# Kernel tuning notes

Measured on AMD Instinct MI355X. Metric: run time of the kernel, lower is better.

## Reference

```python
import jax, jax.numpy as jnp
import numpy as np

B = 4096          # players (batch)
DEG = 64          # asteroids per player
A = B * DEG       # total asteroids
E = A             # one edge per asteroid (asteroid -> its player)
PD, AD, ED = 5, 3, 7
HID = 64
HEADS = 4
OUT = HID         # GATv2Conv out_channels (concat=False -> mean over heads)
L = 2             # num_layers
NEG_SLOPE = 0.2
LN_EPS = 1e-5


def setup_inputs() -> dict:
    key = jax.random.key(0)
    ks = jax.random.split(key, 20)
    f = jnp.float32
    inp = {}
    inp["player_feat"] = jax.random.normal(ks[0], (B, PD), f)
    inp["asteroid_feat"] = jax.random.normal(ks[1], (A, AD), f)
    src = jnp.arange(E, dtype=jnp.int32)
    dst = src // DEG                      # player batch index per edge
    inp["edge_index"] = jnp.stack([src, dst])  # [2, E] int32
    inp["edge_attr"] = jax.random.normal(ks[2], (E, ED), f)
    sc = 0.1
    # input projections
    inp["Wp"] = jax.random.normal(ks[3], (PD, HID), f) * sc
    inp["bp"] = jnp.zeros((HID,), f)
    inp["Wa"] = jax.random.normal(ks[4], (AD, HID), f) * sc
    inp["ba"] = jnp.zeros((HID,), f)
    # per-layer GATv2 params (stacked over L)
    inp["Wl"] = jax.random.normal(ks[5], (L, HID, HEADS * OUT), f) * sc
    inp["bl"] = jnp.zeros((L, HEADS * OUT), f)
    inp["Wr"] = jax.random.normal(ks[6], (L, HID, HEADS * OUT), f) * sc
    inp["br"] = jnp.zeros((L, HEADS * OUT), f)
    inp["We"] = jax.random.normal(ks[7], (L, ED, HEADS * OUT), f) * sc
    inp["att"] = jax.random.normal(ks[8], (L, HEADS, OUT), f) * sc
    inp["bias"] = jnp.zeros((L, OUT), f)
    inp["ln_g"] = jnp.ones((L, HID), f)
    inp["ln_b"] = jnp.zeros((L, HID), f)
    return inp


def _layer_norm(x, g, b):
    mu = jnp.mean(x, axis=-1, keepdims=True)
    var = jnp.mean(jnp.square(x - mu), axis=-1, keepdims=True)
    return (x - mu) * jax.lax.rsqrt(var + LN_EPS) * g + b


def _gatv2(x, src, dst, edge_attr, Wl, bl, Wr, br, We, att, bias, n_nodes):
    # x: [N, HID]; src/dst: [E]; PyG GATv2Conv, add_self_loops=False, concat=False
    xl = (x @ Wl + bl).reshape(-1, HEADS, OUT)   # source transform
    xr = (x @ Wr + br).reshape(-1, HEADS, OUT)   # target transform
    ea = (edge_attr @ We).reshape(-1, HEADS, OUT)
    e = xl[src] + xr[dst] + ea                   # [E, H, O]
    e = jnp.where(e >= 0, e, NEG_SLOPE * e)      # LeakyReLU(0.2)
    logits = jnp.einsum('eho,ho->eh', e, att)    # [E, H]
    # segment softmax over incoming edges of each target node
    m = jax.ops.segment_max(logits, dst, num_segments=n_nodes)
    al = jnp.exp(logits - m[dst])
    den = jax.ops.segment_sum(al, dst, num_segments=n_nodes)
    alpha = al / den[dst]                        # [E, H]
    msg = alpha[:, :, None] * xl[src]            # [E, H, O]
    out = jax.ops.segment_sum(msg, dst, num_segments=n_nodes)  # [N, H, O]
    return jnp.mean(out, axis=1) + bias          # concat=False -> head mean


def reference(player_feat, asteroid_feat, edge_index, edge_attr,
              Wp, bp, Wa, ba, Wl, bl, Wr, br, We, att, bias, ln_g, ln_b):
    batch = player_feat.shape[0]
    h_p = jax.nn.relu(player_feat @ Wp + bp)
    h_a = jax.nn.relu(asteroid_feat @ Wa + ba)
    x = jnp.concatenate([h_p, h_a], axis=0)      # [N, HID]
    n_nodes = x.shape[0]
    src = edge_index[0] + batch                  # asteroid local -> global idx
    dst = edge_index[1]
    for i in range(L):
        x_new = _gatv2(x, src, dst, edge_attr, Wl[i], bl[i], Wr[i], br[i],
                       We[i], att[i], bias[i], n_nodes)
        x = _layer_norm(x + jax.nn.relu(x_new), ln_g[i], ln_b[i])
    return x[:batch]
```

## Files before the change

kernel.cpp:

```cpp
#include <hip/hip_runtime.h>


typedef __bf16 bf16x8 __attribute__((ext_vector_type(8)));
typedef float  f32x4  __attribute__((ext_vector_type(4)));

union FragU { unsigned short u[8]; bf16x8 v; };

__device__ __forceinline__ float bf2f(unsigned short u) {
    union { unsigned int i; float f; } v; v.i = ((unsigned int)u) << 16; return v.f;
}
__device__ __forceinline__ unsigned short f2bf(float f) {
    union { __bf16 b; unsigned short u; } x; x.b = (__bf16)f; return x.u;
}

#define NEG_SLOPE 0.2f
#define LN_EPS 1e-5f
#define XS 88

struct Smem {
    __align__(16) unsigned short xa[2][64 * XS];
    __align__(16) unsigned short xpb[2][64];
    __align__(16) float alf[2][256];
    float outp[2][256];
    float xp[2][64];
    float afs[2][192];
    float rbs[64], gs[64], bs[64];
};

#define WS_NEED (163840 + 3 * 8192)

__global__ __launch_bounds__(256) void prep_weights(
    const float* __restrict__ Wl, const float* __restrict__ Wr,
    const float* __restrict__ We, const float* __restrict__ bl,
    const float* __restrict__ att, const float* __restrict__ br,
    unsigned short* __restrict__ wlf, unsigned short* __restrict__ wrf,
    unsigned short* __restrict__ wef, f32x4* __restrict__ blq,
    f32x4* __restrict__ attq, f32x4* __restrict__ brq)
{
    int s = blockIdx.x * 256 + threadIdx.x;
    {
        int layer = s >> 14, k = (s >> 8) & 63, c = s & 255;
        int jj = k & 7, q = (k >> 3) & 3, ko = k >> 5;
        int nt = (c >> 4) & 3, frag = nt * 2 + ko;
        int t = (c >> 6) * 64 + q * 16 + (c & 15);
        int di = ((layer * 8 + frag) * 256 + t) * 8 + jj;
        wlf[di] = f2bf(Wl[s]);
        wrf[di] = f2bf(Wr[s]);
    }
    int i = s;
    if (i < 16384) {
        int j2 = i & 7, t2 = (i >> 3) & 255, n2 = (i >> 11) & 3, l2 = (i >> 13) & 1;
        int q2 = (t2 >> 4) & 3;
        int c2 = (t2 >> 6) * 64 + n2 * 16 + (t2 & 15);
        wef[i] = (q2 == 0 && j2 < 7) ? f2bf(We[l2 * 1792 + j2 * 256 + c2])
                                     : (unsigned short)0;
    }
    if (i < 512) {
        int lyr = i >> 8, tt = i & 255;
        int hb = (tt >> 6) * 64, mm = tt & 15;
        f32x4 b, a, r;
        #pragma unroll
        for (int n = 0; n < 4; ++n) {
            int cc = hb + n * 16 + mm;
            b[n] = bl[lyr * 256 + cc];
            a[n] = att[lyr * 256 + cc];
            r[n] = br[lyr * 256 + cc];
        }
        blq[i] = b; attq[i] = a; brq[i] = r;
    }
}

template <bool WS>
__global__ __launch_bounds__(256) void gnn_main(
    const float* __restrict__ pf, const float* __restrict__ af,
    const float* __restrict__ eat, const float* __restrict__ Wp,
    const float* __restrict__ bp, const float* __restrict__ Wa,
    const float* __restrict__ ba, const float* __restrict__ Wl,
    const float* __restrict__ bl, const float* __restrict__ Wr,
    const float* __restrict__ br, const float* __restrict__ We,
    const float* __restrict__ att, const float* __restrict__ bias,
    const float* __restrict__ lng, const float* __restrict__ lnb,
    const unsigned short* __restrict__ wlf, const unsigned short* __restrict__ wrf,
    const unsigned short* __restrict__ wef, const f32x4* __restrict__ blq,
    const f32x4* __restrict__ attq, const f32x4* __restrict__ brq,
    float* __restrict__ out)
{
    __shared__ Smem sm;
    const int p0 = blockIdx.x * 2, t = threadIdx.x;
    const int w = t >> 6, l = t & 63, q = l >> 4, m = l & 15;
    const int cbase = w * 64;

    #pragma unroll
    for (int idx = t; idx < 384; idx += 256) {
        int pl = idx >= 192, o = idx - pl * 192;
        sm.afs[pl][o] = af[(p0 + pl) * 192 + o];
    }
    if (t < 64) {
        sm.rbs[t] = fmaxf(bias[t], 0.f);
        sm.gs[t] = lng[t];
        sm.bs[t] = lnb[t];
    }
    if (t < 128) {
        int pl = t >> 6, tt = t & 63;
        float acc = bp[tt];
        #pragma unroll
        for (int d = 0; d < 5; ++d) acc += pf[(p0 + pl) * 5 + d] * Wp[d * 64 + tt];
        float xp0 = fmaxf(acc, 0.f);
        sm.xp[pl][tt] = xp0;
        sm.xpb[pl][tt] = f2bf(xp0);
    }
    __syncthreads();
    {
        const int pl = w >> 1, rbase = (w & 1) * 32, k = l;
        float wa0 = Wa[k], wa1 = Wa[64 + k], wa2 = Wa[128 + k], bak = ba[k];
        #pragma unroll
        for (int rep = 0; rep < 32; ++rep) {
            int j = rbase + rep;
            float acc = bak + sm.afs[pl][j * 3] * wa0 + sm.afs[pl][j * 3 + 1] * wa1
                      + sm.afs[pl][j * 3 + 2] * wa2;
            sm.xa[pl][j * XS + k] = f2bf(fmaxf(acc, 0.f));
        }
    }
    #pragma unroll
    for (int idx = t; idx < 1024; idx += 256) {
        int pl = idx >> 9, jd = idx & 511, j = jd >> 3, d = jd & 7;
        sm.xa[pl][j * XS + 64 + d] = (d < 7) ? f2bf(eat[((p0 + pl) * 64 + j) * 7 + d])
                                             : (unsigned short)0;
    }
    __syncthreads();

    for (int layer = 0; layer < 2; ++layer) {
        f32x4 blv, atv, brv;
        if constexpr (WS) {
            blv = blq[layer * 256 + t];
            atv = attq[layer * 256 + t];
            brv = brq[layer * 256 + t];
        } else {
            #pragma unroll
            for (int nt = 0; nt < 4; ++nt) {
                int c = cbase + nt * 16 + m;
                blv[nt] = bl[layer * 256 + c];
                atv[nt] = att[layer * 256 + c];
                brv[nt] = br[layer * 256 + c];
            }
        }

        float xrc[2][4];
        {
            FragU xf0[2], xf1[2];
            #pragma unroll
            for (int pl = 0; pl < 2; ++pl) {
                xf0[pl].v = *reinterpret_cast<const bf16x8*>(&sm.xpb[pl][q * 8]);
                xf1[pl].v = *reinterpret_cast<const bf16x8*>(&sm.xpb[pl][32 + q * 8]);
            }
            #pragma unroll
            for (int nt = 0; nt < 4; ++nt) {
                FragU r0, r1;
                if constexpr (WS) {
                    r0.v = *reinterpret_cast<const bf16x8*>(&wrf[((layer * 8 + nt * 2 + 0) * 256 + t) * 8]);
                    r1.v = *reinterpret_cast<const bf16x8*>(&wrf[((layer * 8 + nt * 2 + 1) * 256 + t) * 8]);
                } else {
                    int c = cbase + nt * 16 + m;
                    #pragma unroll
                    for (int jj = 0; jj < 8; ++jj) {
                        r0.u[jj] = f2bf(Wr[layer * 16384 + (q * 8 + jj) * 256 + c]);
                        r1.u[jj] = f2bf(Wr[layer * 16384 + (32 + q * 8 + jj) * 256 + c]);
                    }
                }
                #pragma unroll
                for (int pl = 0; pl < 2; ++pl) {
                    f32x4 cx = { brv[nt], brv[nt], brv[nt], brv[nt] };
                    cx = __builtin_amdgcn_mfma_f32_16x16x32_bf16(xf0[pl].v, r0.v, cx, 0, 0, 0);
                    cx = __builtin_amdgcn_mfma_f32_16x16x32_bf16(xf1[pl].v, r1.v, cx, 0, 0, 0);
                    xrc[pl][nt] = cx[0];
                }
            }
        }

        FragU bfr[8];
        bf16x8 ebf[4];
        if constexpr (WS) {
            #pragma unroll
            for (int f = 0; f < 8; ++f)
                bfr[f].v = *reinterpret_cast<const bf16x8*>(&wlf[((layer * 8 + f) * 256 + t) * 8]);
            #pragma unroll
            for (int nt = 0; nt < 4; ++nt)
                ebf[nt] = *reinterpret_cast<const bf16x8*>(&wef[((layer * 4 + nt) * 256 + t) * 8]);
        } else {
            const float* Wli = Wl + layer * 16384;
            #pragma unroll
            for (int nt = 0; nt < 4; ++nt) {
                int c = cbase + nt * 16 + m;
                #pragma unroll
                for (int ko = 0; ko < 2; ++ko) {
                    int kb = ko * 32 + q * 8;
                    #pragma unroll
                    for (int jj = 0; jj < 8; ++jj)
                        bfr[nt * 2 + ko].u[jj] = f2bf(Wli[(kb + jj) * 256 + c]);
                }
                FragU e;
                #pragma unroll
                for (int jj = 0; jj < 8; ++jj)
                    e.u[jj] = (q == 0 && jj < 7) ? f2bf(We[layer * 1792 + jj * 256 + c])
                                                 : (unsigned short)0;
                ebf[nt] = e.v;
            }
        }

        float bx[2][4];
        #pragma unroll
        for (int pl = 0; pl < 2; ++pl)
            #pragma unroll
            for (int nt = 0; nt < 4; ++nt) bx[pl][nt] = blv[nt] + xrc[pl][nt];

        const bool b0 = (m & 1) != 0, b1 = (m & 2) != 0;
        const bool b2 = (m & 4) != 0, b3 = (m & 8) != 0;
        float P[2][4];
        #pragma unroll
        for (int mt = 0; mt < 4; ++mt) {
            const int row = mt * 16 + m;
            #pragma unroll
            for (int pl = 0; pl < 2; ++pl) {
                bf16x8 a0 = *reinterpret_cast<const bf16x8*>(&sm.xa[pl][row * XS + q * 8]);
                bf16x8 a1 = *reinterpret_cast<const bf16x8*>(&sm.xa[pl][row * XS + 32 + q * 8]);
                bf16x8 a2 = *reinterpret_cast<const bf16x8*>(&sm.xa[pl][row * XS + 64]);
                float lp4[4] = { 0.f, 0.f, 0.f, 0.f };
                #pragma unroll
                for (int nt = 0; nt < 4; ++nt) {
                    f32x4 acc = { bx[pl][nt], bx[pl][nt], bx[pl][nt], bx[pl][nt] };
                    acc = __builtin_amdgcn_mfma_f32_16x16x32_bf16(a0, bfr[nt * 2 + 0].v, acc, 0, 0, 0);
                    acc = __builtin_amdgcn_mfma_f32_16x16x32_bf16(a1, bfr[nt * 2 + 1].v, acc, 0, 0, 0);
                    f32x4 ef = __builtin_amdgcn_mfma_f32_16x16x32_bf16(a2, ebf[nt], acc, 0, 0, 0);
                    #pragma unroll
                    for (int r = 0; r < 4; ++r) {
                        float ev = ef[r];
                        ev = fmaxf(ev, NEG_SLOPE * ev);
                        lp4[r] += ev * atv[nt];
                    }
                }
                float e0k = b0 ? lp4[1] : lp4[0], e0s = b0 ? lp4[0] : lp4[1];
                float ea = e0k + __shfl_xor(e0s, 1, 64);
                float e1k = b0 ? lp4[3] : lp4[2], e1s = b0 ? lp4[2] : lp4[3];
                float eb = e1k + __shfl_xor(e1s, 1, 64);
                float fk = b1 ? eb : ea, fs = b1 ? ea : eb;
                P[pl][mt] = fk + __shfl_xor(fs, 2, 64);
            }
        }

        float rden[2];
        #pragma unroll
        for (int pl = 0; pl < 2; ++pl) {
            float g0k = b2 ? P[pl][1] : P[pl][0], g0s = b2 ? P[pl][0] : P[pl][1];
            float ga = g0k + __shfl_xor(g0s, 4, 64);
            float g1k = b2 ? P[pl][3] : P[pl][2], g1s = b2 ? P[pl][2] : P[pl][3];
            float gb = g1k + __shfl_xor(g1s, 4, 64);
            float hk = b3 ? gb : ga, hs = b3 ? ga : gb;
            float lg = hk + __shfl_xor(hs, 8, 64);
            float al = __expf(lg);
            float den = al;
            #pragma unroll
            for (int msk = 1; msk <= 32; msk <<= 1) den += __shfl_xor(den, msk, 64);
            rden[pl] = 1.f / den;
            const int rj = ((m >> 2) * 16) + (q * 4) + (m & 3);
            sm.alf[pl][w * 64 + rj] = al;
        }
        __builtin_amdgcn_wave_barrier();

        #pragma unroll
        for (int pl = 0; pl < 2; ++pl) {
            const f32x4* alv = reinterpret_cast<const f32x4*>(&sm.alf[pl][cbase]);
            f32x4 al4[4];
            #pragma unroll
            for (int mt = 0; mt < 4; ++mt) al4[mt] = alv[mt * 4 + q];
            float s[4] = { 0.f, 0.f, 0.f, 0.f };
            #pragma unroll
            for (int mt = 0; mt < 4; ++mt) {
                const int row = mt * 16 + m;
                bf16x8 a0 = *reinterpret_cast<const bf16x8*>(&sm.xa[pl][row * XS + q * 8]);
                bf16x8 a1 = *reinterpret_cast<const bf16x8*>(&sm.xa[pl][row * XS + 32 + q * 8]);
                #pragma unroll
                for (int nt = 0; nt < 4; ++nt) {
                    f32x4 c1 = { bx[pl][nt], bx[pl][nt], bx[pl][nt], bx[pl][nt] };
                    c1 = __builtin_amdgcn_mfma_f32_16x16x32_bf16(a0, bfr[nt * 2 + 0].v, c1, 0, 0, 0);
                    c1 = __builtin_amdgcn_mfma_f32_16x16x32_bf16(a1, bfr[nt * 2 + 1].v, c1, 0, 0, 0);
                    s[nt] += al4[mt][0] * c1[0] + al4[mt][1] * c1[1]
                           + al4[mt][2] * c1[2] + al4[mt][3] * c1[3];
                }
            }
            #pragma unroll
            for (int nt = 0; nt < 4; ++nt) {
                float sv = s[nt];
                sv += __shfl_xor(sv, 16, 64);
                sv += __shfl_xor(sv, 32, 64);
                if (q == 0) sm.outp[pl][cbase + nt * 16 + m] = sv * rden[pl] - xrc[pl][nt];
            }
        }
        __syncthreads();

        if (layer == 0) {
            {
                const int g = t >> 1, pl = g >> 6, j = g & 63, part = t & 1;
                unsigned short* rowp = &sm.xa[pl][j * XS + part * 32];
                FragU A0, A1, A2, A3;
                A0.v = *reinterpret_cast<const bf16x8*>(rowp);
                A1.v = *reinterpret_cast<const bf16x8*>(rowp + 8);
                A2.v = *reinterpret_cast<const bf16x8*>(rowp + 16);
                A3.v = *reinterpret_cast<const bf16x8*>(rowp + 24);
                float v[32], sum = 0.f, sq = 0.f;
                #pragma unroll
                for (int i = 0; i < 32; ++i) {
                    unsigned short us = (i < 8) ? A0.u[i] : (i < 16) ? A1.u[i - 8]
                                      : (i < 24) ? A2.u[i - 16] : A3.u[i - 24];
                    float x = bf2f(us) + sm.rbs[part * 32 + i];
                    v[i] = x; sum += x; sq += x * x;
                }
                sum += __shfl_xor(sum, 1, 64); sq += __shfl_xor(sq, 1, 64);
                float mu = sum * (1.f / 64.f);
                float var = sq * (1.f / 64.f) - mu * mu;
                float rs = rsqrtf(var + LN_EPS);
                FragU O0, O1, O2, O3;
                #pragma unroll
                for (int i = 0; i < 32; ++i) {
                    int col = part * 32 + i;
                    unsigned short ub = f2bf((v[i] - mu) * rs * sm.gs[col] + sm.bs[col]);
                    if (i < 8) O0.u[i] = ub;
                    else if (i < 16) O1.u[i - 8] = ub;
                    else if (i < 24) O2.u[i - 16] = ub;
                    else O3.u[i - 24] = ub;
                }
                *reinterpret_cast<bf16x8*>(rowp) = O0.v;
                *reinterpret_cast<bf16x8*>(rowp + 8) = O1.v;
                *reinterpret_cast<bf16x8*>(rowp + 16) = O2.v;
                *reinterpret_cast<bf16x8*>(rowp + 24) = O3.v;
            }
            if (t < 128) {
                const int pl = t >> 6, tt = t & 63;
                float xnew = 0.25f * (sm.outp[pl][tt] + sm.outp[pl][64 + tt]
                                    + sm.outp[pl][128 + tt] + sm.outp[pl][192 + tt])
                           + bias[tt];
                float v = sm.xp[pl][tt] + fmaxf(xnew, 0.f);
                float sum = v, sq = v * v;
                #pragma unroll
                for (int msk = 1; msk <= 32; msk <<= 1) {
                    sum += __shfl_xor(sum, msk, 64);
                    sq  += __shfl_xor(sq,  msk, 64);
                }
                float mu = sum * (1.f / 64.f);
                float var = sq * (1.f / 64.f) - mu * mu;
                float y = (v - mu) * rsqrtf(var + LN_EPS) * lng[tt] + lnb[tt];
                sm.xp[pl][tt] = y;
                sm.xpb[pl][tt] = f2bf(y);
            }
            __syncthreads();
        } else {
            if (t < 128) {
                const int pl = t >> 6, tt = t & 63;
                float xnew = 0.25f * (sm.outp[pl][tt] + sm.outp[pl][64 + tt]
                                    + sm.outp[pl][128 + tt] + sm.outp[pl][192 + tt])
                           + bias[64 + tt];
                float v = sm.xp[pl][tt] + fmaxf(xnew, 0.f);
                float sum = v, sq = v * v;
                #pragma unroll
                for (int msk = 1; msk <= 32; msk <<= 1) {
                    sum += __shfl_xor(sum, msk, 64);
                    sq  += __shfl_xor(sq,  msk, 64);
                }
                float mu = sum * (1.f / 64.f);
                float var = sq * (1.f / 64.f) - mu * mu;
                float y = (v - mu) * rsqrtf(var + LN_EPS) * lng[64 + tt] + lnb[64 + tt];
                out[(p0 + pl) * 64 + tt] = y;
            }
        }
    }
}

extern "C" void kernel_launch(void* const* d_in, const int* in_sizes, int n_in,
                              void* d_out, int out_size, void* d_ws, size_t ws_size,
                              hipStream_t stream) {
    const float* pf   = (const float*)d_in[0];
    const float* af   = (const float*)d_in[1];
    const float* eat  = (const float*)d_in[3];
    const float* Wp   = (const float*)d_in[4];
    const float* bp   = (const float*)d_in[5];
    const float* Wa   = (const float*)d_in[6];
    const float* ba   = (const float*)d_in[7];
    const float* Wl   = (const float*)d_in[8];
    const float* bl   = (const float*)d_in[9];
    const float* Wr   = (const float*)d_in[10];
    const float* br   = (const float*)d_in[11];
    const float* We   = (const float*)d_in[12];
    const float* att  = (const float*)d_in[13];
    const float* bias = (const float*)d_in[14];
    const float* lng  = (const float*)d_in[15];
    const float* lnb  = (const float*)d_in[16];
    float* out = (float*)d_out;

    const int B = in_sizes[0] / 5;
    unsigned short* wlf = (unsigned short*)d_ws;
    unsigned short* wrf = wlf + 32768;
    unsigned short* wef = wrf + 32768;
    f32x4* blq  = (f32x4*)((char*)d_ws + 163840);
    f32x4* attq = blq + 512;
    f32x4* brq  = attq + 512;

    if (ws_size >= WS_NEED) {
        prep_weights<<<dim3(128), dim3(256), 0, stream>>>(
            Wl, Wr, We, bl, att, br, wlf, wrf, wef, blq, attq, brq);
        gnn_main<true><<<dim3(B / 2), dim3(256), 0, stream>>>(
            pf, af, eat, Wp, bp, Wa, ba, Wl, bl, Wr, br, We, att, bias, lng, lnb,
            wlf, wrf, wef, blq, attq, brq, out);
    } else {
        gnn_main<false><<<dim3(B / 2), dim3(256), 0, stream>>>(
            pf, af, eat, Wp, bp, Wa, ba, Wl, bl, Wr, br, We, att, bias, lng, lnb,
            wlf, wrf, wef, blq, attq, brq, out);
    }
}
```

Before: 166.0 us.

## Process four players per block to amortize weight fragment loads

Each block now handles four players instead of two, so every weight fragment loaded from global memory feeds twice as many MFMA tiles, and the grid halves to B/4 blocks. The shared-memory row stride drops from 88 to 72, the per-row layer norm is done by one thread over 64 columns instead of two threads over 32, and launch bounds request 3 blocks per CU. In exchange, register pressure rises (64-float arrays, 4x4 accumulators), shared memory per block doubles, and the new stride may change LDS bank conflicts.

```diff
diff --git a/kernel.cpp b/kernel.cpp
--- a/kernel.cpp
+++ b/kernel.cpp
@@ -15,15 +15,15 @@
 
 #define NEG_SLOPE 0.2f
 #define LN_EPS 1e-5f
-#define XS 88
+#define XS 72
 
 struct Smem {
-    __align__(16) unsigned short xa[2][64 * XS];
-    __align__(16) unsigned short xpb[2][64];
-    __align__(16) float alf[2][256];
-    float outp[2][256];
-    float xp[2][64];
-    float afs[2][192];
+    __align__(16) unsigned short xa[4][64 * XS];
+    __align__(16) unsigned short xpb[4][64];
+    __align__(16) float alf[4][256];
+    float outp[4][256];
+    float xp[4][64];
+    float afs[4][192];
     float rbs[64], gs[64], bs[64];
 };
 
@@ -71,7 +71,7 @@
 }
 
 template <bool WS>
-__global__ __launch_bounds__(256) void gnn_main(
+__global__ __launch_bounds__(256, 3) void gnn_main(
     const float* __restrict__ pf, const float* __restrict__ af,
     const float* __restrict__ eat, const float* __restrict__ Wp,
     const float* __restrict__ bp, const float* __restrict__ Wa,
@@ -86,13 +86,14 @@
     float* __restrict__ out)
 {
     __shared__ Smem sm;
-    const int p0 = blockIdx.x * 2, t = threadIdx.x;
+    const int p0 = blockIdx.x * 4, t = threadIdx.x;
     const int w = t >> 6, l = t & 63, q = l >> 4, m = l & 15;
     const int cbase = w * 64;
 
     #pragma unroll
-    for (int idx = t; idx < 384; idx += 256) {
-        int pl = idx >= 192, o = idx - pl * 192;
+    for (int it = 0; it < 3; ++it) {
+        int idx = it * 256 + t;
+        int pl = idx / 192, o = idx - pl * 192;
         sm.afs[pl][o] = af[(p0 + pl) * 192 + o];
     }
     if (t < 64) {
@@ -100,8 +101,8 @@
         sm.gs[t] = lng[t];
         sm.bs[t] = lnb[t];
     }
-    if (t < 128) {
-        int pl = t >> 6, tt = t & 63;
+    {
+        int pl = w, tt = l;
         float acc = bp[tt];
         #pragma unroll
         for (int d = 0; d < 5; ++d) acc += pf[(p0 + pl) * 5 + d] * Wp[d * 64 + tt];
@@ -111,18 +112,18 @@
     }
     __syncthreads();
     {
-        const int pl = w >> 1, rbase = (w & 1) * 32, k = l;
+        const int pl = w, k = l;
         float wa0 = Wa[k], wa1 = Wa[64 + k], wa2 = Wa[128 + k], bak = ba[k];
         #pragma unroll
-        for (int rep = 0; rep < 32; ++rep) {
-            int j = rbase + rep;
+        for (int j = 0; j < 64; ++j) {
             float acc = bak + sm.afs[pl][j * 3] * wa0 + sm.afs[pl][j * 3 + 1] * wa1
                       + sm.afs[pl][j * 3 + 2] * wa2;
             sm.xa[pl][j * XS + k] = f2bf(fmaxf(acc, 0.f));
         }
     }
     #pragma unroll
-    for (int idx = t; idx < 1024; idx += 256) {
+    for (int it = 0; it < 8; ++it) {
+        int idx = it * 256 + t;
         int pl = idx >> 9, jd = idx & 511, j = jd >> 3, d = jd & 7;
         sm.xa[pl][j * XS + 64 + d] = (d < 7) ? f2bf(eat[((p0 + pl) * 64 + j) * 7 + d])
                                              : (unsigned short)0;
@@ -145,11 +146,11 @@
             }
         }
 
-        float xrc[2][4];
+        float bx[4][4];
         {
-            FragU xf0[2], xf1[2];
-            #pragma unroll
-            for (int pl = 0; pl < 2; ++pl) {
+            FragU xf0[4], xf1[4];
+            #pragma unroll
+            for (int pl = 0; pl < 4; ++pl) {
                 xf0[pl].v = *reinterpret_cast<const bf16x8*>(&sm.xpb[pl][q * 8]);
                 xf1[pl].v = *reinterpret_cast<const bf16x8*>(&sm.xpb[pl][32 + q * 8]);
             }
@@ -168,11 +169,11 @@
                     }
                 }
                 #pragma unroll
-                for (int pl = 0; pl < 2; ++pl) {
+                for (int pl = 0; pl < 4; ++pl) {
                     f32x4 cx = { brv[nt], brv[nt], brv[nt], brv[nt] };
                     cx = __builtin_amdgcn_mfma_f32_16x16x32_bf16(xf0[pl].v, r0.v, cx, 0, 0, 0);
                     cx = __builtin_amdgcn_mfma_f32_16x16x32_bf16(xf1[pl].v, r1.v, cx, 0, 0, 0);
-                    xrc[pl][nt] = cx[0];
+                    bx[pl][nt] = blv[nt] + cx[0];
                 }
             }
         }
@@ -207,20 +208,14 @@
             }
         }
 
-        float bx[2][4];
-        #pragma unroll
-        for (int pl = 0; pl < 2; ++pl)
-            #pragma unroll
-            for (int nt = 0; nt < 4; ++nt) bx[pl][nt] = blv[nt] + xrc[pl][nt];
-
         const bool b0 = (m & 1) != 0, b1 = (m & 2) != 0;
         const bool b2 = (m & 4) != 0, b3 = (m & 8) != 0;
-        float P[2][4];
+        float P[4][4];
         #pragma unroll
         for (int mt = 0; mt < 4; ++mt) {
             const int row = mt * 16 + m;
             #pragma unroll
-            for (int pl = 0; pl < 2; ++pl) {
+            for (int pl = 0; pl < 4; ++pl) {
                 bf16x8 a0 = *reinterpret_cast<const bf16x8*>(&sm.xa[pl][row * XS + q * 8]);
                 bf16x8 a1 = *reinterpret_cast<const bf16x8*>(&sm.xa[pl][row * XS + 32 + q * 8]);
                 bf16x8 a2 = *reinterpret_cast<const bf16x8*>(&sm.xa[pl][row * XS + 64]);
@@ -247,9 +242,9 @@
             }
         }
 
-        float rden[2];
-        #pragma unroll
-        for (int pl = 0; pl < 2; ++pl) {
+        float rden[4];
+        #pragma unroll
+        for (int pl = 0; pl < 4; ++pl) {
             float g0k = b2 ? P[pl][1] : P[pl][0], g0s = b2 ? P[pl][0] : P[pl][1];
             float ga = g0k + __shfl_xor(g0s, 4, 64);
             float g1k = b2 ? P[pl][3] : P[pl][2], g1s = b2 ? P[pl][2] : P[pl][3];
@@ -267,7 +262,7 @@
         __builtin_amdgcn_wave_barrier();
 
         #pragma unroll
-        for (int pl = 0; pl < 2; ++pl) {
+        for (int pl = 0; pl < 4; ++pl) {
             const f32x4* alv = reinterpret_cast<const f32x4*>(&sm.alf[pl][cbase]);
             f32x4 al4[4];
             #pragma unroll
@@ -292,49 +287,42 @@
                 float sv = s[nt];
                 sv += __shfl_xor(sv, 16, 64);
                 sv += __shfl_xor(sv, 32, 64);
-                if (q == 0) sm.outp[pl][cbase + nt * 16 + m] = sv * rden[pl] - xrc[pl][nt];
+                if (q == 0)
+                    sm.outp[pl][cbase + nt * 16 + m] = sv * rden[pl] - (bx[pl][nt] - blv[nt]);
             }
         }
         __syncthreads();
 
         if (layer == 0) {
             {
-                const int g = t >> 1, pl = g >> 6, j = g & 63, part = t & 1;
-                unsigned short* rowp = &sm.xa[pl][j * XS + part * 32];
-                FragU A0, A1, A2, A3;
-                A0.v = *reinterpret_cast<const bf16x8*>(rowp);
-                A1.v = *reinterpret_cast<const bf16x8*>(rowp + 8);
-                A2.v = *reinterpret_cast<const bf16x8*>(rowp + 16);
-                A3.v = *reinterpret_cast<const bf16x8*>(rowp + 24);
-                float v[32], sum = 0.f, sq = 0.f;
-                #pragma unroll
-                for (int i = 0; i < 32; ++i) {
-                    unsigned short us = (i < 8) ? A0.u[i] : (i < 16) ? A1.u[i - 8]
-                                      : (i < 24) ? A2.u[i - 16] : A3.u[i - 24];
-                    float x = bf2f(us) + sm.rbs[part * 32 + i];
+                const int pl = t >> 6, j = t & 63;
+                unsigned short* rowp = &sm.xa[pl][j * XS];
+                FragU A[8];
+                #pragma unroll
+                for (int f = 0; f < 8; ++f)
+                    A[f].v = *reinterpret_cast<const bf16x8*>(rowp + f * 8);
+                float v[64], sum = 0.f, sq = 0.f;
+                #pragma unroll
+                for (int i = 0; i < 64; ++i) {
+                    float x = bf2f(A[i >> 3].u[i & 7]) + sm.rbs[i];
                     v[i] = x; sum += x; sq += x * x;
                 }
-                sum += __shfl_xor(sum, 1, 64); sq += __shfl_xor(sq, 1, 64);
                 float mu = sum * (1.f / 64.f);
                 float var = sq * (1.f / 64.f) - mu * mu;
                 float rs = rsqrtf(var + LN_EPS);
-                FragU O0, O1, O2, O3;
-                #pragma unroll
-                for (int i = 0; i < 32; ++i) {
-                    int col = part * 32 + i;
-                    unsigned short ub = f2bf((v[i] - mu) * rs * sm.gs[col] + sm.bs[col]);
-                    if (i < 8) O0.u[i] = ub;
-                    else if (i < 16) O1.u[i - 8] = ub;
-                    else if (i < 24) O2.u[i - 16] = ub;
-                    else O3.u[i - 24] = ub;
-                }
-                *reinterpret_cast<bf16x8*>(rowp) = O0.v;
-                *reinterpret_cast<bf16x8*>(rowp + 8) = O1.v;
-                *reinterpret_cast<bf16x8*>(rowp + 16) = O2.v;
-                *reinterpret_cast<bf16x8*>(rowp + 24) = O3.v;
-            }
-            if (t < 128) {
-                const int pl = t >> 6, tt = t & 63;
+                #pragma unroll
+                for (int f = 0; f < 8; ++f) {
+                    FragU O;
+                    #pragma unroll
+                    for (int k = 0; k < 8; ++k) {
+                        int col = f * 8 + k;
+                        O.u[k] = f2bf((v[col] - mu) * rs * sm.gs[col] + sm.bs[col]);
+                    }
+                    *reinterpret_cast<bf16x8*>(rowp + f * 8) = O.v;
+                }
+            }
+            {
+                const int pl = w, tt = l;
                 float xnew = 0.25f * (sm.outp[pl][tt] + sm.outp[pl][64 + tt]
                                     + sm.outp[pl][128 + tt] + sm.outp[pl][192 + tt])
                            + bias[tt];
@@ -353,8 +341,8 @@
             }
             __syncthreads();
         } else {
-            if (t < 128) {
-                const int pl = t >> 6, tt = t & 63;
+            {
+                const int pl = w, tt = l;
                 float xnew = 0.25f * (sm.outp[pl][tt] + sm.outp[pl][64 + tt]
                                     + sm.outp[pl][128 + tt] + sm.outp[pl][192 + tt])
                            + bias[64 + tt];
@@ -406,11 +394,11 @@
     if (ws_size >= WS_NEED) {
         prep_weights<<<dim3(128), dim3(256), 0, stream>>>(
             Wl, Wr, We, bl, att, br, wlf, wrf, wef, blq, attq, brq);
-        gnn_main<true><<<dim3(B / 2), dim3(256), 0, stream>>>(
+        gnn_main<true><<<dim3(B / 4), dim3(256), 0, stream>>>(
             pf, af, eat, Wp, bp, Wa, ba, Wl, bl, Wr, br, We, att, bias, lng, lnb,
             wlf, wrf, wef, blq, attq, brq, out);
     } else {
-        gnn_main<false><<<dim3(B / 2), dim3(256), 0, stream>>>(
+        gnn_main<false><<<dim3(B / 4), dim3(256), 0, stream>>>(
             pf, af, eat, Wp, bp, Wa, ba, Wl, bl, Wr, br, We, att, bias, lng, lnb,
             wlf, wrf, wef, blq, attq, brq, out);
     }
```

Result: slower. 179.0 us (+7.9%).
